# Kernel tuning notes

Hardware: AMD Instinct MI355X
Metric: run time of the kernel (lower is better)

The kernel has to match this reference:

```python
import jax, jax.numpy as jnp
import numpy as np

K_ORDER = 3
GRID_N = 10
GRID_LO, GRID_HI = -2.0, 2.0
LAYERS = [(49, 256), (256, 256), (256, 10)]
NCOEF = GRID_N + K_ORDER  # 13


def mish(x):
    return x * jnp.tanh(jax.nn.softplus(x))


def bspline_basis(x):
    # x: (B, in) -> basis (B, in, GRID_N + K_ORDER)
    h = (GRID_HI - GRID_LO) / GRID_N
    knots = GRID_LO + h * jnp.arange(-K_ORDER, GRID_N + K_ORDER + 1, dtype=x.dtype)  # (G+2k+1,)
    xx = x[..., None]
    B = ((xx >= knots[:-1]) & (xx < knots[1:])).astype(x.dtype)  # degree-0, (B,in,G+2k)
    for d in range(1, K_ORDER + 1):
        left = (xx - knots[: -(d + 1)]) / (knots[d:-1] - knots[: -(d + 1)]) * B[..., :-1]
        right = (knots[d + 1:] - xx) / (knots[d + 1:] - knots[1:-d]) * B[..., 1:]
        B = left + right
    return B  # (B, in, G+k)


def kan_layer(x, coef, scale_base, scale_sp, bias):
    # x: (B,in); coef: (in,out,G+k); scales: (in,out); bias: (out,)
    basis = bspline_basis(x)                                   # (B,in,G+k)
    spline = jnp.einsum('big,iog->bo', basis, coef * scale_sp[..., None])
    base = jnp.einsum('bi,io->bo', mish(x), scale_base)
    return base + spline + bias


def setup_inputs() -> dict:
    key = jax.random.key(0)
    ks = jax.random.split(key, 1 + 4 * len(LAYERS))
    inp = {'x': jax.random.normal(ks[0], (8192, 1, 28, 28), dtype=jnp.float32)}
    i = 1
    for li, (fin, fout) in enumerate(LAYERS, start=1):
        inp[f'coef{li}'] = 0.1 * jax.random.normal(ks[i], (fin, fout, NCOEF), dtype=jnp.float32); i += 1
        inp[f'sb{li}'] = 1.0 + 0.1 * jax.random.normal(ks[i], (fin, fout), dtype=jnp.float32); i += 1
        inp[f'sp{li}'] = 1.0 + 0.1 * jax.random.normal(ks[i], (fin, fout), dtype=jnp.float32); i += 1
        inp[f'b{li}'] = jnp.zeros((fout,), dtype=jnp.float32); i += 1
    return inp


def reference(x, coef1, sb1, sp1, b1, coef2, sb2, sp2, b2, coef3, sb3, sp3, b3):
    B = x.shape[0]
    # avg_pool2d(x, 4): 28x28 -> 7x7
    h = x.reshape(B, 1, 7, 4, 7, 4).mean(axis=(3, 5))
    h = h.reshape(B, 49)
    h = kan_layer(h, coef1, sb1, sp1, b1)
    h = kan_layer(h, coef2, sb2, sp2, b2)
    h = kan_layer(h, coef3, sb3, sp3, b3)
    return jax.nn.log_softmax(h, axis=1)
```

## Files before the change

kernel.cpp:

```cpp
#include <hip/hip_runtime.h>
#include <hip/hip_bf16.h>

typedef __bf16 bf16x8_t __attribute__((ext_vector_type(8)));
typedef float f32x4_t __attribute__((ext_vector_type(4)));
using bf16 = __hip_bfloat16;

__device__ __forceinline__ unsigned short f2bf_bits(float v) {
  __hip_bfloat16 h = __float2bfloat16(v);
  return *reinterpret_cast<unsigned short*>(&h);
}

__device__ __forceinline__ float mish_f(float x) {
  float z = __expf(x);
  float n = z * (z + 2.0f);
  float m = x * n / (n + 2.0f);
  return (x > 10.0f) ? x : m;
}

__device__ __forceinline__ void kan_feats28(bf16* dst, float x) {
  unsigned int* d32 = (unsigned int*)dst;
#pragma unroll
  for (int d = 0; d < 7; ++d) d32[d] = 0u;
  float t = (x + 3.2f) * 2.5f;
  if (t >= 0.0f && t < 16.0f) {
    float tf = floorf(t);
    int c = (int)tf;
    float u = t - tf;
    float um = 1.0f - u;
    float u2 = u * u, u3 = u2 * u;
    const float s6 = 1.0f / 6.0f;
    float w0 = um * um * um * s6;
    float w1 = (3.0f * u3 - 6.0f * u2 + 4.0f) * s6;
    float w2 = (-3.0f * u3 + 3.0f * u2 + 3.0f * u + 1.0f) * s6;
    float w3 = u3 * s6;
    int j0 = c - 3;
    if (j0 >= 0)               dst[j0]     = __float2bfloat16(w0);
    if (j0 >= -1 && j0 <= 11)  dst[j0 + 1] = __float2bfloat16(w1);
    if (j0 >= -2 && j0 <= 10)  dst[j0 + 2] = __float2bfloat16(w2);
    if (j0 <= 9)               dst[j0 + 3] = __float2bfloat16(w3);
  }
  dst[13] = __float2bfloat16(mish_f(x));
}

__global__ __launch_bounds__(256) void prep_all(
    const float* __restrict__ c1, const float* __restrict__ sb1, const float* __restrict__ sp1,
    const float* __restrict__ c2, const float* __restrict__ sb2, const float* __restrict__ sp2,
    const float* __restrict__ c3, const float* __restrict__ sb3, const float* __restrict__ sp3,
    bf16* __restrict__ W1f, bf16* __restrict__ W2f, bf16* __restrict__ W3f) {
  const int b = blockIdx.x, t = threadIdx.x;
  float vals[14];
  if (b < 49) {
    const int i = b, o = t;
    const int ntg = o >> 4, lrr = o & 15;
    const size_t io = (size_t)i * 256 + o;
    const float spv = sp1[io];
#pragma unroll
    for (int r = 0; r < 13; ++r) vals[r] = c1[io * 13 + r] * spv;
    vals[13] = sb1[io];
#pragma unroll
    for (int d = 0; d < 7; ++d) {
      const int k2 = i * 14 + 2 * d;
      const int s = k2 >> 5, r2 = k2 & 31;
      const size_t off = ((size_t)(s * 16 + ntg)) * 512 + lrr * 32 + (r2 >> 3) * 8 + (r2 & 7);
      *(unsigned int*)(W1f + off) = (unsigned int)f2bf_bits(vals[2 * d]) |
                                    ((unsigned int)f2bf_bits(vals[2 * d + 1]) << 16);
    }
  } else if (b == 49) {
    const int ntg = t >> 4, lrr = t & 15;
#pragma unroll
    for (int d = 0; d < 9; ++d) {
      const int k2 = 686 + 2 * d;
      const int r2 = k2 & 31;
      *(unsigned int*)(W1f + ((size_t)(21 * 16 + ntg)) * 512 + lrr * 32 + (r2 >> 3) * 8 + (r2 & 7)) = 0u;
    }
  } else if (b < 306) {
    const int i = b - 50;
    const int o = t;
    const int ntg = o >> 4, lrr = o & 15;
    const size_t io = (size_t)i * 256 + o;
    const float spv = sp2[io];
#pragma unroll
    for (int r = 0; r < 13; ++r) vals[r] = c2[io * 13 + r] * spv;
    vals[13] = sb2[io];
#pragma unroll
    for (int d = 0; d < 7; ++d) {
      const int k2 = i * 14 + 2 * d;
      const int s = k2 >> 5, r2 = k2 & 31;
      const size_t off = ((size_t)(s * 16 + ntg)) * 512 + lrr * 32 + (r2 >> 3) * 8 + (r2 & 7);
      *(unsigned int*)(W2f + off) = (unsigned int)f2bf_bits(vals[2 * d]) |
                                    ((unsigned int)f2bf_bits(vals[2 * d + 1]) << 16);
    }
  } else {
    const int idx = (b - 306) * 256 + t;
    const int i = idx >> 4, o = idx & 15;
    if (o < 10) {
      const size_t io = (size_t)i * 10 + o;
      const float spv = sp3[io];
#pragma unroll
      for (int r = 0; r < 13; ++r) vals[r] = c3[io * 13 + r] * spv;
      vals[13] = sb3[io];
#pragma unroll
      for (int d = 0; d < 7; ++d) {
        const int k2 = i * 14 + 2 * d;
        const int s = k2 >> 5, r2 = k2 & 31;
        const size_t off = (size_t)s * 512 + o * 32 + (r2 >> 3) * 8 + (r2 & 7);
        *(unsigned int*)(W3f + off) = (unsigned int)f2bf_bits(vals[2 * d]) |
                                      ((unsigned int)f2bf_bits(vals[2 * d + 1]) << 16);
      }
    } else {
#pragma unroll
      for (int d = 0; d < 7; ++d) {
        const int k2 = i * 14 + 2 * d;
        const int s = k2 >> 5, r2 = k2 & 31;
        *(unsigned int*)(W3f + (size_t)s * 512 + o * 32 + (r2 >> 3) * 8 + (r2 & 7)) = 0u;
      }
    }
  }
}

__global__ __launch_bounds__(1024, 4) void meganet(
    const float* __restrict__ x, const bf16* __restrict__ W1f,
    const bf16* __restrict__ W2f, const bf16* __restrict__ W3f,
    const float* __restrict__ b1, const float* __restrict__ b2,
    const float* __restrict__ b3, float* __restrict__ out) {
  __shared__ __align__(16) char lds[104448];
  float* const Hs = (float*)lds;
  bf16* const A0 = (bf16*)(lds + 36864);
  bf16* const A1 = (bf16*)(lds + 67072);
  float* const P = (float*)(lds + 97280);
  float* const xs = (float*)lds;
  float* const Red = (float*)(lds + 36864);
  float* const V = (float*)(lds + 67072);

  const int t = threadIdx.x;
  const int w = t >> 6, lane = t & 63, quad = lane >> 4, lr = lane & 15;
  const int tr = (t >> 4) & 31, ej = t & 15;
  const int r0 = blockIdx.x * 32;
  const int foff = lr * 32 + quad * 8;
  const bool cons = (w < 8);
  const int ntg0 = 2 * w;

  for (int h = 0; h < 2; ++h) {
    const float4* src = (const float4*)x + (size_t)(r0 + h * 16) * 196;
    float4* xd = (float4*)xs;
#pragma unroll
    for (int l = 0; l < 4; ++l) {
      const int idx = t + l * 1024;
      if (idx < 3136) xd[idx] = src[idx];
    }
    __syncthreads();
    if (t < 784) {
      const int img = t / 49, p = t - img * 49;
      const int oh = p / 7, ow = p - oh * 7;
      const float* xi = xs + img * 784 + oh * 112 + ow * 4;
      f32x4_t s4 = (f32x4_t){0.f, 0.f, 0.f, 0.f};
#pragma unroll
      for (int rr = 0; rr < 4; ++rr) {
        const f32x4_t v = *(const f32x4_t*)(xi + rr * 28);
        s4 += v;
      }
      P[(h * 16 + img) * 56 + p] = (s4[0] + s4[1] + s4[2] + s4[3]) * (1.0f / 16.0f);
    }
    __syncthreads();
  }

  f32x4_t acc[2][2];
#pragma unroll
  for (int m = 0; m < 2; ++m)
#pragma unroll
    for (int n = 0; n < 2; ++n) acc[m][n] = (f32x4_t){0.f, 0.f, 0.f, 0.f};

  bf16* const Bch0 = A0;
  bf16* const Bch1 = A1;
  bf16x8_t q0[4], q1[4];
  if (cons) {
#pragma unroll
    for (int s = 0; s < 4; ++s) {
      q0[s] = *(const bf16x8_t*)(W1f + (size_t)(s * 16 + ntg0) * 512 + foff);
      q1[s] = *(const bf16x8_t*)(W1f + (size_t)(s * 16 + ntg0 + 1) * 512 + foff);
    }
  } else {
    kan_feats28(Bch0 + tr * 232 + ej * 14, P[tr * 56 + ej]);
  }
  __syncthreads();
#pragma unroll
  for (int c = 0; c < 4; ++c) {
    const bf16* const Ac = (c & 1) ? Bch1 : Bch0;
    bf16* const An = (c & 1) ? Bch0 : Bch1;
    if (cons) {
      const int nks = (c < 3) ? 7 : 1;
#pragma unroll
      for (int ks = 0; ks < 7; ++ks) {
        if (ks >= nks) continue;
        const int kk = c * 7 + ks;
        const int sl = kk & 3;
        bf16x8_t bb0 = q0[sl], bb1 = q1[sl];
        if (kk + 4 < 22) {
          q0[sl] = *(const bf16x8_t*)(W1f + (size_t)((kk + 4) * 16 + ntg0) * 512 + foff);
          q1[sl] = *(const bf16x8_t*)(W1f + (size_t)((kk + 4) * 16 + ntg0 + 1) * 512 + foff);
        }
#pragma unroll
        for (int m = 0; m < 2; ++m) {
          bf16x8_t a = *(const bf16x8_t*)(Ac + (m * 16 + lr) * 232 + ks * 32 + quad * 8);
          acc[m][0] = __builtin_amdgcn_mfma_f32_16x16x32_bf16(a, bb0, acc[m][0], 0, 0, 0);
          acc[m][1] = __builtin_amdgcn_mfma_f32_16x16x32_bf16(a, bb1, acc[m][1], 0, 0, 0);
        }
      }
    } else {
      if (c < 2) {
        kan_feats28(An + tr * 232 + ej * 14, P[tr * 56 + (c + 1) * 16 + ej]);
      } else if (c == 2) {
        if (ej == 0) kan_feats28(An + tr * 232, P[tr * 56 + 48]);
        else if (ej == 1) {
          unsigned int* z = (unsigned int*)(An + tr * 232 + 14);
#pragma unroll
          for (int d = 0; d < 9; ++d) z[d] = 0u;
        }
      }
    }
    __syncthreads();
  }
  if (cons) {
#pragma unroll
    for (int m = 0; m < 2; ++m)
#pragma unroll
      for (int n = 0; n < 2; ++n) {
        const int col = w * 32 + n * 16 + lr;
        const float bn = b1[col];
        f32x4_t v;
#pragma unroll
        for (int r = 0; r < 4; ++r) v[r] = acc[m][n][r] + bn;
        *(f32x4_t*)(Hs + col * 36 + m * 16 + quad * 4) = v;
      }
  }
  __syncthreads();

#pragma unroll
  for (int m = 0; m < 2; ++m)
#pragma unroll
    for (int n = 0; n < 2; ++n) acc[m][n] = (f32x4_t){0.f, 0.f, 0.f, 0.f};
  if (cons) {
#pragma unroll
    for (int s = 0; s < 4; ++s) {
      q0[s] = *(const bf16x8_t*)(W2f + (size_t)(s * 16 + ntg0) * 512 + foff);
      q1[s] = *(const bf16x8_t*)(W2f + (size_t)(s * 16 + ntg0 + 1) * 512 + foff);
    }
  } else {
    kan_feats28(A0 + tr * 472 + ej * 14, Hs[ej * 36 + tr]);
    kan_feats28(A0 + tr * 472 + (16 + ej) * 14, Hs[(16 + ej) * 36 + tr]);
  }
  __syncthreads();
#pragma unroll
  for (int S = 0; S < 8; ++S) {
    const bf16* const Ac = (S & 1) ? A1 : A0;
    bf16* const An = (S & 1) ? A0 : A1;
    if (cons) {
#pragma unroll
      for (int ks = 0; ks < 14; ++ks) {
        const int kk = S * 14 + ks;
        const int sl = kk & 3;
        bf16x8_t bb0 = q0[sl], bb1 = q1[sl];
        if (kk + 4 < 112) {
          q0[sl] = *(const bf16x8_t*)(W2f + (size_t)((kk + 4) * 16 + ntg0) * 512 + foff);
          q1[sl] = *(const bf16x8_t*)(W2f + (size_t)((kk + 4) * 16 + ntg0 + 1) * 512 + foff);
        }
#pragma unroll
        for (int m = 0; m < 2; ++m) {
          bf16x8_t a = *(const bf16x8_t*)(Ac + (m * 16 + lr) * 472 + ks * 32 + quad * 8);
          acc[m][0] = __builtin_amdgcn_mfma_f32_16x16x32_bf16(a, bb0, acc[m][0], 0, 0, 0);
          acc[m][1] = __builtin_amdgcn_mfma_f32_16x16x32_bf16(a, bb1, acc[m][1], 0, 0, 0);
        }
      }
    } else if (S < 7) {
      const int col = 32 * (S + 1);
      kan_feats28(An + tr * 472 + ej * 14, Hs[(col + ej) * 36 + tr]);
      kan_feats28(An + tr * 472 + (16 + ej) * 14, Hs[(col + 16 + ej) * 36 + tr]);
    }
    __syncthreads();
  }
  if (cons) {
#pragma unroll
    for (int m = 0; m < 2; ++m)
#pragma unroll
      for (int n = 0; n < 2; ++n) {
        const int col = w * 32 + n * 16 + lr;
        const float bn = b2[col];
        f32x4_t v;
#pragma unroll
        for (int r = 0; r < 4; ++r) v[r] = acc[m][n][r] + bn;
        *(f32x4_t*)(Hs + col * 36 + m * 16 + quad * 4) = v;
      }
  }
  __syncthreads();

  f32x4_t acc3[2];
  acc3[0] = (f32x4_t){0.f, 0.f, 0.f, 0.f};
  acc3[1] = acc3[0];
  bf16x8_t q3[4];
  if (w < 7) {
#pragma unroll
    for (int s = 0; s < 4; ++s)
      q3[s] = *(const bf16x8_t*)(W3f + (size_t)(s * 7 + w) * 512 + foff);
  } else if (!cons) {
    kan_feats28(A0 + tr * 472 + ej * 14, Hs[ej * 36 + tr]);
    kan_feats28(A0 + tr * 472 + (16 + ej) * 14, Hs[(16 + ej) * 36 + tr]);
  }
  __syncthreads();
#pragma unroll
  for (int S = 0; S < 8; ++S) {
    const bf16* const Ac = (S & 1) ? A1 : A0;
    bf16* const An = (S & 1) ? A0 : A1;
    if (w < 7) {
      {
        const int c0 = 2 * S;
        bf16x8_t bb = q3[c0 & 3];
        if (c0 + 4 < 16)
          q3[c0 & 3] = *(const bf16x8_t*)(W3f + (size_t)((c0 + 4) * 7 + w) * 512 + foff);
        bf16x8_t a0 = *(const bf16x8_t*)(Ac + lr * 472 + w * 32 + quad * 8);
        bf16x8_t a1 = *(const bf16x8_t*)(Ac + (16 + lr) * 472 + w * 32 + quad * 8);
        acc3[0] = __builtin_amdgcn_mfma_f32_16x16x32_bf16(a0, bb, acc3[0], 0, 0, 0);
        acc3[1] = __builtin_amdgcn_mfma_f32_16x16x32_bf16(a1, bb, acc3[1], 0, 0, 0);
      }
      {
        const int c1 = 2 * S + 1;
        bf16x8_t bb = q3[c1 & 3];
        if (c1 + 4 < 16)
          q3[c1 & 3] = *(const bf16x8_t*)(W3f + (size_t)((c1 + 4) * 7 + w) * 512 + foff);
        bf16x8_t a0 = *(const bf16x8_t*)(Ac + lr * 472 + (w + 7) * 32 + quad * 8);
        bf16x8_t a1 = *(const bf16x8_t*)(Ac + (16 + lr) * 472 + (w + 7) * 32 + quad * 8);
        acc3[0] = __builtin_amdgcn_mfma_f32_16x16x32_bf16(a0, bb, acc3[0], 0, 0, 0);
        acc3[1] = __builtin_amdgcn_mfma_f32_16x16x32_bf16(a1, bb, acc3[1], 0, 0, 0);
      }
    } else if (!cons && S < 7) {
      const int col = 32 * (S + 1);
      kan_feats28(An + tr * 472 + ej * 14, Hs[(col + ej) * 36 + tr]);
      kan_feats28(An + tr * 472 + (16 + ej) * 14, Hs[(col + 16 + ej) * 36 + tr]);
    }
    __syncthreads();
  }
  if (w < 7) {
#pragma unroll
    for (int m = 0; m < 2; ++m)
#pragma unroll
      for (int r = 0; r < 4; ++r)
        Red[w * 512 + (m * 16 + quad * 4 + r) * 16 + lr] = acc3[m][r];
  }
  __syncthreads();
  if (t < 512) {
    float s = (ej < 10) ? b3[ej] : 0.f;
#pragma unroll
    for (int ks = 0; ks < 7; ++ks) s += Red[ks * 512 + tr * 16 + ej];
    V[tr * 16 + ej] = s;
  }
  __syncthreads();
  if (t < 32) {
    float vv[10];
#pragma unroll
    for (int o = 0; o < 10; ++o) vv[o] = V[t * 16 + o];
    float mx = vv[0];
#pragma unroll
    for (int o = 1; o < 10; ++o) mx = fmaxf(mx, vv[o]);
    float se = 0.f;
#pragma unroll
    for (int o = 0; o < 10; ++o) se += expf(vv[o] - mx);
    const float l = mx + logf(se);
#pragma unroll
    for (int o = 0; o < 10; ++o) out[(size_t)(r0 + t) * 10 + o] = vv[o] - l;
  }
}

extern "C" void kernel_launch(void* const* d_in, const int* in_sizes, int n_in,
                              void* d_out, int out_size, void* d_ws, size_t ws_size,
                              hipStream_t stream) {
  const float* x = (const float*)d_in[0];
  const float* coef1 = (const float*)d_in[1];
  const float* sb1 = (const float*)d_in[2];
  const float* sp1 = (const float*)d_in[3];
  const float* b1 = (const float*)d_in[4];
  const float* coef2 = (const float*)d_in[5];
  const float* sb2 = (const float*)d_in[6];
  const float* sp2 = (const float*)d_in[7];
  const float* b2 = (const float*)d_in[8];
  const float* coef3 = (const float*)d_in[9];
  const float* sb3 = (const float*)d_in[10];
  const float* sp3 = (const float*)d_in[11];
  const float* b3 = (const float*)d_in[12];
  float* out = (float*)d_out;

  char* ws = (char*)d_ws;
  bf16* W1f = (bf16*)ws;
  bf16* W2f = (bf16*)(ws + 360448);
  bf16* W3f = (bf16*)(ws + 2195456);

  prep_all<<<322, 256, 0, stream>>>(coef1, sb1, sp1, coef2, sb2, sp2,
                                    coef3, sb3, sp3, W1f, W2f, W3f);
  meganet<<<256, 1024, 0, stream>>>(x, W1f, W2f, W3f, b1, b2, b3, out);
}
```

Measured before the change: 138.4 us.

## Halve rows per block to double grid size and fill more CUs

Each block now handles 16 batch rows instead of 32, so the grid doubles from 256 to 512 blocks and the LDS footprint roughly halves. MFMA tiles drop from two M-tiles to one, and the feature-generation threads are remapped to cover 32 columns per row in a single pass. With 256 CUs, the old 256-block grid gave at most one block per CU. The new layout aims for better CU coverage and latency hiding, at the cost of loading each weight fragment from L2 twice as often per row.

```diff
diff --git a/kernel.cpp b/kernel.cpp
--- a/kernel.cpp
+++ b/kernel.cpp
@@ -118,30 +118,32 @@
   }
 }
 
-__global__ __launch_bounds__(1024, 4) void meganet(
+__global__ __launch_bounds__(1024, 8) void meganet(
     const float* __restrict__ x, const bf16* __restrict__ W1f,
     const bf16* __restrict__ W2f, const bf16* __restrict__ W3f,
     const float* __restrict__ b1, const float* __restrict__ b2,
     const float* __restrict__ b3, float* __restrict__ out) {
-  __shared__ __align__(16) char lds[104448];
+  __shared__ __align__(16) char lds[53760];
   float* const Hs = (float*)lds;
-  bf16* const A0 = (bf16*)(lds + 36864);
-  bf16* const A1 = (bf16*)(lds + 67072);
-  float* const P = (float*)(lds + 97280);
+  bf16* const A0 = (bf16*)(lds + 20480);
+  bf16* const A1 = (bf16*)(lds + 35584);
+  float* const P = (float*)(lds + 50176);
   float* const xs = (float*)lds;
-  float* const Red = (float*)(lds + 36864);
-  float* const V = (float*)(lds + 67072);
+  float* const Red = (float*)(lds + 20480);
+  float* const V = (float*)(lds + 35584);
 
   const int t = threadIdx.x;
   const int w = t >> 6, lane = t & 63, quad = lane >> 4, lr = lane & 15;
-  const int tr = (t >> 4) & 31, ej = t & 15;
-  const int r0 = blockIdx.x * 32;
+  const int pr = t & 511;
+  const int tr = pr >> 4, ej = pr & 15;
+  const int trc = pr >> 5, cj = pr & 31;
+  const int r0 = blockIdx.x * 16;
   const int foff = lr * 32 + quad * 8;
   const bool cons = (w < 8);
   const int ntg0 = 2 * w;
 
-  for (int h = 0; h < 2; ++h) {
-    const float4* src = (const float4*)x + (size_t)(r0 + h * 16) * 196;
+  {
+    const float4* src = (const float4*)x + (size_t)r0 * 196;
     float4* xd = (float4*)xs;
 #pragma unroll
     for (int l = 0; l < 4; ++l) {
@@ -159,16 +161,14 @@
         const f32x4_t v = *(const f32x4_t*)(xi + rr * 28);
         s4 += v;
       }
-      P[(h * 16 + img) * 56 + p] = (s4[0] + s4[1] + s4[2] + s4[3]) * (1.0f / 16.0f);
-    }
-    __syncthreads();
-  }
-
-  f32x4_t acc[2][2];
-#pragma unroll
-  for (int m = 0; m < 2; ++m)
-#pragma unroll
-    for (int n = 0; n < 2; ++n) acc[m][n] = (f32x4_t){0.f, 0.f, 0.f, 0.f};
+      P[img * 56 + p] = (s4[0] + s4[1] + s4[2] + s4[3]) * (1.0f / 16.0f);
+    }
+    __syncthreads();
+  }
+
+  f32x4_t acc[2];
+  acc[0] = (f32x4_t){0.f, 0.f, 0.f, 0.f};
+  acc[1] = acc[0];
 
   bf16* const Bch0 = A0;
   bf16* const Bch1 = A1;
@@ -179,7 +179,7 @@
       q0[s] = *(const bf16x8_t*)(W1f + (size_t)(s * 16 + ntg0) * 512 + foff);
       q1[s] = *(const bf16x8_t*)(W1f + (size_t)(s * 16 + ntg0 + 1) * 512 + foff);
     }
-  } else {
+  } else if (pr < 256) {
     kan_feats28(Bch0 + tr * 232 + ej * 14, P[tr * 56 + ej]);
   }
   __syncthreads();
@@ -199,14 +199,11 @@
           q0[sl] = *(const bf16x8_t*)(W1f + (size_t)((kk + 4) * 16 + ntg0) * 512 + foff);
           q1[sl] = *(const bf16x8_t*)(W1f + (size_t)((kk + 4) * 16 + ntg0 + 1) * 512 + foff);
         }
-#pragma unroll
-        for (int m = 0; m < 2; ++m) {
-          bf16x8_t a = *(const bf16x8_t*)(Ac + (m * 16 + lr) * 232 + ks * 32 + quad * 8);
-          acc[m][0] = __builtin_amdgcn_mfma_f32_16x16x32_bf16(a, bb0, acc[m][0], 0, 0, 0);
-          acc[m][1] = __builtin_amdgcn_mfma_f32_16x16x32_bf16(a, bb1, acc[m][1], 0, 0, 0);
-        }
-      }
-    } else {
+        bf16x8_t a = *(const bf16x8_t*)(Ac + lr * 232 + ks * 32 + quad * 8);
+        acc[0] = __builtin_amdgcn_mfma_f32_16x16x32_bf16(a, bb0, acc[0], 0, 0, 0);
+        acc[1] = __builtin_amdgcn_mfma_f32_16x16x32_bf16(a, bb1, acc[1], 0, 0, 0);
+      }
+    } else if (pr < 256) {
       if (c < 2) {
         kan_feats28(An + tr * 232 + ej * 14, P[tr * 56 + (c + 1) * 16 + ej]);
       } else if (c == 2) {
@@ -222,23 +219,19 @@
   }
   if (cons) {
 #pragma unroll
-    for (int m = 0; m < 2; ++m)
-#pragma unroll
-      for (int n = 0; n < 2; ++n) {
-        const int col = w * 32 + n * 16 + lr;
-        const float bn = b1[col];
-        f32x4_t v;
-#pragma unroll
-        for (int r = 0; r < 4; ++r) v[r] = acc[m][n][r] + bn;
-        *(f32x4_t*)(Hs + col * 36 + m * 16 + quad * 4) = v;
-      }
-  }
-  __syncthreads();
-
-#pragma unroll
-  for (int m = 0; m < 2; ++m)
-#pragma unroll
-    for (int n = 0; n < 2; ++n) acc[m][n] = (f32x4_t){0.f, 0.f, 0.f, 0.f};
+    for (int n = 0; n < 2; ++n) {
+      const int col = w * 32 + n * 16 + lr;
+      const float bn = b1[col];
+      f32x4_t v;
+#pragma unroll
+      for (int r = 0; r < 4; ++r) v[r] = acc[n][r] + bn;
+      *(f32x4_t*)(Hs + col * 20 + quad * 4) = v;
+    }
+  }
+  __syncthreads();
+
+  acc[0] = (f32x4_t){0.f, 0.f, 0.f, 0.f};
+  acc[1] = acc[0];
   if (cons) {
 #pragma unroll
     for (int s = 0; s < 4; ++s) {
@@ -246,8 +239,7 @@
       q1[s] = *(const bf16x8_t*)(W2f + (size_t)(s * 16 + ntg0 + 1) * 512 + foff);
     }
   } else {
-    kan_feats28(A0 + tr * 472 + ej * 14, Hs[ej * 36 + tr]);
-    kan_feats28(A0 + tr * 472 + (16 + ej) * 14, Hs[(16 + ej) * 36 + tr]);
+    kan_feats28(A0 + trc * 472 + cj * 14, Hs[cj * 20 + trc]);
   }
   __syncthreads();
 #pragma unroll
@@ -264,46 +256,37 @@
           q0[sl] = *(const bf16x8_t*)(W2f + (size_t)((kk + 4) * 16 + ntg0) * 512 + foff);
           q1[sl] = *(const bf16x8_t*)(W2f + (size_t)((kk + 4) * 16 + ntg0 + 1) * 512 + foff);
         }
-#pragma unroll
-        for (int m = 0; m < 2; ++m) {
-          bf16x8_t a = *(const bf16x8_t*)(Ac + (m * 16 + lr) * 472 + ks * 32 + quad * 8);
-          acc[m][0] = __builtin_amdgcn_mfma_f32_16x16x32_bf16(a, bb0, acc[m][0], 0, 0, 0);
-          acc[m][1] = __builtin_amdgcn_mfma_f32_16x16x32_bf16(a, bb1, acc[m][1], 0, 0, 0);
-        }
+        bf16x8_t a = *(const bf16x8_t*)(Ac + lr * 472 + ks * 32 + quad * 8);
+        acc[0] = __builtin_amdgcn_mfma_f32_16x16x32_bf16(a, bb0, acc[0], 0, 0, 0);
+        acc[1] = __builtin_amdgcn_mfma_f32_16x16x32_bf16(a, bb1, acc[1], 0, 0, 0);
       }
     } else if (S < 7) {
       const int col = 32 * (S + 1);
-      kan_feats28(An + tr * 472 + ej * 14, Hs[(col + ej) * 36 + tr]);
-      kan_feats28(An + tr * 472 + (16 + ej) * 14, Hs[(col + 16 + ej) * 36 + tr]);
+      kan_feats28(An + trc * 472 + cj * 14, Hs[(col + cj) * 20 + trc]);
     }
     __syncthreads();
   }
   if (cons) {
 #pragma unroll
-    for (int m = 0; m < 2; ++m)
-#pragma unroll
-      for (int n = 0; n < 2; ++n) {
-        const int col = w * 32 + n * 16 + lr;
-        const float bn = b2[col];
-        f32x4_t v;
-#pragma unroll
-        for (int r = 0; r < 4; ++r) v[r] = acc[m][n][r] + bn;
-        *(f32x4_t*)(Hs + col * 36 + m * 16 + quad * 4) = v;
-      }
-  }
-  __syncthreads();
-
-  f32x4_t acc3[2];
-  acc3[0] = (f32x4_t){0.f, 0.f, 0.f, 0.f};
-  acc3[1] = acc3[0];
+    for (int n = 0; n < 2; ++n) {
+      const int col = w * 32 + n * 16 + lr;
+      const float bn = b2[col];
+      f32x4_t v;
+#pragma unroll
+      for (int r = 0; r < 4; ++r) v[r] = acc[n][r] + bn;
+      *(f32x4_t*)(Hs + col * 20 + quad * 4) = v;
+    }
+  }
+  __syncthreads();
+
+  f32x4_t acc3 = (f32x4_t){0.f, 0.f, 0.f, 0.f};
   bf16x8_t q3[4];
   if (w < 7) {
 #pragma unroll
     for (int s = 0; s < 4; ++s)
       q3[s] = *(const bf16x8_t*)(W3f + (size_t)(s * 7 + w) * 512 + foff);
   } else if (!cons) {
-    kan_feats28(A0 + tr * 472 + ej * 14, Hs[ej * 36 + tr]);
-    kan_feats28(A0 + tr * 472 + (16 + ej) * 14, Hs[(16 + ej) * 36 + tr]);
+    kan_feats28(A0 + trc * 472 + cj * 14, Hs[cj * 20 + trc]);
   }
   __syncthreads();
 #pragma unroll
@@ -316,44 +299,38 @@
         bf16x8_t bb = q3[c0 & 3];
         if (c0 + 4 < 16)
           q3[c0 & 3] = *(const bf16x8_t*)(W3f + (size_t)((c0 + 4) * 7 + w) * 512 + foff);
-        bf16x8_t a0 = *(const bf16x8_t*)(Ac + lr * 472 + w * 32 + quad * 8);
-        bf16x8_t a1 = *(const bf16x8_t*)(Ac + (16 + lr) * 472 + w * 32 + quad * 8);
-        acc3[0] = __builtin_amdgcn_mfma_f32_16x16x32_bf16(a0, bb, acc3[0], 0, 0, 0);
-        acc3[1] = __builtin_amdgcn_mfma_f32_16x16x32_bf16(a1, bb, acc3[1], 0, 0, 0);
+        bf16x8_t a = *(const bf16x8_t*)(Ac + lr * 472 + w * 32 + quad * 8);
+        acc3 = __builtin_amdgcn_mfma_f32_16x16x32_bf16(a, bb, acc3, 0, 0, 0);
       }
       {
         const int c1 = 2 * S + 1;
         bf16x8_t bb = q3[c1 & 3];
         if (c1 + 4 < 16)
           q3[c1 & 3] = *(const bf16x8_t*)(W3f + (size_t)((c1 + 4) * 7 + w) * 512 + foff);
-        bf16x8_t a0 = *(const bf16x8_t*)(Ac + lr * 472 + (w + 7) * 32 + quad * 8);
-        bf16x8_t a1 = *(const bf16x8_t*)(Ac + (16 + lr) * 472 + (w + 7) * 32 + quad * 8);
-        acc3[0] = __builtin_amdgcn_mfma_f32_16x16x32_bf16(a0, bb, acc3[0], 0, 0, 0);
-        acc3[1] = __builtin_amdgcn_mfma_f32_16x16x32_bf16(a1, bb, acc3[1], 0, 0, 0);
+        bf16x8_t a = *(const bf16x8_t*)(Ac + lr * 472 + (w + 7) * 32 + quad * 8);
+        acc3 = __builtin_amdgcn_mfma_f32_16x16x32_bf16(a, bb, acc3, 0, 0, 0);
       }
     } else if (!cons && S < 7) {
       const int col = 32 * (S + 1);
-      kan_feats28(An + tr * 472 + ej * 14, Hs[(col + ej) * 36 + tr]);
-      kan_feats28(An + tr * 472 + (16 + ej) * 14, Hs[(col + 16 + ej) * 36 + tr]);
+      kan_feats28(An + trc * 472 + cj * 14, Hs[(col + cj) * 20 + trc]);
     }
     __syncthreads();
   }
   if (w < 7) {
 #pragma unroll
-    for (int m = 0; m < 2; ++m)
-#pragma unroll
-      for (int r = 0; r < 4; ++r)
-        Red[w * 512 + (m * 16 + quad * 4 + r) * 16 + lr] = acc3[m][r];
-  }
-  __syncthreads();
-  if (t < 512) {
-    float s = (ej < 10) ? b3[ej] : 0.f;
-#pragma unroll
-    for (int ks = 0; ks < 7; ++ks) s += Red[ks * 512 + tr * 16 + ej];
-    V[tr * 16 + ej] = s;
-  }
-  __syncthreads();
-  if (t < 32) {
+    for (int r = 0; r < 4; ++r)
+      Red[w * 256 + (quad * 4 + r) * 16 + lr] = acc3[r];
+  }
+  __syncthreads();
+  if (t < 256) {
+    const int rr = t >> 4, oj = t & 15;
+    float s = (oj < 10) ? b3[oj] : 0.f;
+#pragma unroll
+    for (int ks = 0; ks < 7; ++ks) s += Red[ks * 256 + rr * 16 + oj];
+    V[rr * 16 + oj] = s;
+  }
+  __syncthreads();
+  if (t < 16) {
     float vv[10];
 #pragma unroll
     for (int o = 0; o < 10; ++o) vv[o] = V[t * 16 + o];
@@ -394,5 +371,5 @@
 
   prep_all<<<322, 256, 0, stream>>>(coef1, sb1, sp1, coef2, sb2, sp2,
                                     coef3, sb3, sp3, W1f, W2f, W3f);
-  meganet<<<256, 1024, 0, stream>>>(x, W1f, W2f, W3f, b1, b2, b3, out);
-}
+  meganet<<<512, 1024, 0, stream>>>(x, W1f, W2f, W3f, b1, b2, b3, out);
+}
```

After: 205.7 us. +48.6%, slower.
